# Performance work log

Hardware: AMD Instinct MI355X
Metric: run time of the kernel (lower is better)

## Reference

```python
import jax, jax.numpy as jnp
import numpy as np

N, E, B = 65536, 524288, 256
FEAT, EMB, NH, NB, NC = 64, 128, 4, 2, 4
OUT = EMB // NH
SLOPE = 0.01  # LeakyReLU negative_slope used everywhere in the module


def lrelu(x):
    return jnp.where(x > 0, x, SLOPE * x)


def seg_softmax(logits, seg, nseg, mask):
    # PyG softmax(src, batch): exp(x - segment_max) / (segment_sum + 1e-16)
    z = jnp.where(mask, logits, -jnp.inf)
    m = jax.ops.segment_max(z, seg, num_segments=nseg)
    m = jnp.where(jnp.isfinite(m), m, 0.0)
    e = jnp.exp(z - m[seg])
    s = jax.ops.segment_sum(e, seg, num_segments=nseg)
    return e / (s[seg] + 1e-16)


def topk_pool(x, seg, w, min_score, nseg):
    # PyG TopKPooling with min_score: score = softmax(x.w, batch);
    # keep nodes with score > min(min_score, per-graph max - 1e-7); x_out = x*score.
    score = x @ w  # [N]
    sm = seg_softmax(score, seg, nseg, jnp.ones(score.shape, bool))
    smax = jax.ops.segment_max(sm, seg, num_segments=nseg)
    thr = jnp.minimum(smax - 1e-7, min_score)
    keep = sm > thr[seg]
    xp = jnp.where(keep[:, None], x * sm[:, None], 0.0)
    return xp, keep


def graph_conv_max(x, src, dst, emask, Wrel, Wroot, b, n):
    # PyG GraphConv(aggr='max'): out = Wrel @ max_{j in N(i)} x_j + Wroot @ x_i + b
    msg = jnp.where(emask[:, None], x[src], -jnp.inf)  # [E, d]
    agg = jax.ops.segment_max(msg, dst, num_segments=n)
    agg = jnp.where(jnp.isfinite(agg), agg, 0.0)  # nodes with no in-edges -> 0 (PyG scatter fill)
    return agg @ Wrel.T + x @ Wroot.T + b


def batchnorm(x, g, b):
    # training-mode BatchNorm1d: batch statistics, biased variance, eps=1e-5
    mu = x.mean(0)
    var = x.var(0)
    return g * (x - mu) * jax.lax.rsqrt(var + 1e-5) + b


def setup_inputs() -> dict:
    key = jax.random.key(0)
    ks = jax.random.split(key, 16)
    s_feat = np.float32(1.0 / np.sqrt(FEAT))
    s_emb = np.float32(1.0 / np.sqrt(EMB))
    return {
        "x": jax.random.normal(ks[0], (N, FEAT), jnp.float32),
        "edge_index": jax.random.randint(ks[1], (2, E), 0, N, jnp.int32),
        "batch": (jnp.arange(N, dtype=jnp.int32) // (N // B)).astype(jnp.int32),
        "W_rel0": jax.random.normal(ks[2], (EMB, FEAT), jnp.float32) * s_feat,
        "W_root0": jax.random.normal(ks[3], (EMB, FEAT), jnp.float32) * s_feat,
        "b0": jnp.zeros((EMB,), jnp.float32),
        "bn0_g": jnp.ones((EMB,), jnp.float32),
        "bn0_b": jnp.zeros((EMB,), jnp.float32),
        "blk_pool_w": jax.random.normal(ks[4], (NB, NH, EMB), jnp.float32) * s_emb,
        "blk_Wrel": jax.random.normal(ks[5], (NB, NH, OUT, EMB), jnp.float32) * s_emb,
        "blk_Wroot": jax.random.normal(ks[6], (NB, NH, OUT, EMB), jnp.float32) * s_emb,
        "blk_b": jnp.zeros((NB, NH, OUT), jnp.float32),
        "blk_bn_g": jnp.ones((NB, EMB), jnp.float32),
        "blk_bn_b": jnp.zeros((NB, EMB), jnp.float32),
        "cls_pool_w": jax.random.normal(ks[7], (NC, EMB), jnp.float32) * s_emb,
        "cls_gW1": jax.random.normal(ks[8], (NC, EMB, EMB), jnp.float32) * s_emb,
        "cls_gb1": jnp.zeros((NC, EMB), jnp.float32),
        "cls_gW2": jax.random.normal(ks[9], (NC, EMB), jnp.float32) * s_emb,
        "cls_gb2": jnp.zeros((NC,), jnp.float32),
        "cls_fW1": jax.random.normal(ks[10], (NC, EMB, EMB), jnp.float32) * s_emb,
        "cls_fb1": jnp.zeros((NC, EMB), jnp.float32),
        "cls_fW2": jax.random.normal(ks[11], (NC, EMB), jnp.float32) * s_emb,
        "cls_fb2": jnp.zeros((NC,), jnp.float32),
        "batch_size": B,
    }


def reference(x, edge_index, batch, W_rel0, W_root0, b0, bn0_g, bn0_b,
              blk_pool_w, blk_Wrel, blk_Wroot, blk_b, blk_bn_g, blk_bn_b,
              cls_pool_w, cls_gW1, cls_gb1, cls_gW2, cls_gb2,
              cls_fW1, cls_fb1, cls_fW2, cls_fb2, batch_size):
    n = x.shape[0]
    src, dst = edge_index[0], edge_index[1]
    all_e = jnp.ones(src.shape, bool)
    # conv0 -> leaky_relu -> bn0
    h = lrelu(graph_conv_max(x, src, dst, all_e, W_rel0, W_root0, b0, n))
    cur = batchnorm(h, bn0_g, bn0_b)
    # multi-head blocks: pool (min_score=0.7) -> GraphConv(max) per head, scatter
    # back to original node slots, concat heads, bn, residual 0.5*(x + 0.5*bn(new))
    for bi in range(NB):
        heads = []
        for hi in range(NH):
            xp, keep = topk_pool(cur, batch, blk_pool_w[bi, hi], 0.7, batch_size)
            emask = keep[src] & keep[dst]
            o = lrelu(graph_conv_max(xp, src, dst, emask,
                                     blk_Wrel[bi, hi], blk_Wroot[bi, hi],
                                     blk_b[bi, hi], n))
            heads.append(jnp.where(keep[:, None], o, 0.0))
        new = batchnorm(jnp.concatenate(heads, axis=-1), blk_bn_g[bi], blk_bn_b[bi])
        cur = 0.5 * (cur + 0.5 * new)
    # classification heads: pool (min_score=0.8) -> GlobalAttention -> MLP -> 1
    outs = []
    for c in range(NC):
        xp, keep = topk_pool(cur, batch, cls_pool_w[c], 0.8, batch_size)
        gate = lrelu(xp @ cls_gW1[c].T + cls_gb1[c]) @ cls_gW2[c] + cls_gb2[c]  # [N]
        a = seg_softmax(gate, batch, batch_size, keep)
        pooled = jax.ops.segment_sum(a[:, None] * xp, batch, num_segments=batch_size)  # [B, EMB]
        y = lrelu(pooled @ cls_fW1[c].T + cls_fb1[c]) @ cls_fW2[c] + cls_fb2[c]  # [B]
        outs.append(y)
    logits = jnp.stack(outs, axis=-1)  # [B, NC]
    return jax.nn.log_softmax(logits, axis=-1)
```

## Files before the change

kernel.cpp:

```cpp
#include <hip/hip_runtime.h>
#include <math.h>

#define NN 65536
#define NE 524288
#define NG 256
#define SLOPE 0.01f
#define CAP 131072

__device__ __forceinline__ float lrelu(float v){ return v > 0.f ? v : SLOPE*v; }

__device__ __forceinline__ float blockMax4(float v, float* s4){
  #pragma unroll
  for(int o=32;o>0;o>>=1) v = fmaxf(v, __shfl_down(v, o, 64));
  int t = threadIdx.x;
  __syncthreads();
  if((t&63)==0) s4[t>>6] = v;
  __syncthreads();
  return fmaxf(fmaxf(s4[0], s4[1]), fmaxf(s4[2], s4[3]));
}
__device__ __forceinline__ float blockSum4(float v, float* s4){
  #pragma unroll
  for(int o=32;o>0;o>>=1) v += __shfl_down(v, o, 64);
  int t = threadIdx.x;
  __syncthreads();
  if((t&63)==0) s4[t>>6] = v;
  __syncthreads();
  return (s4[0]+s4[1])+(s4[2]+s4[3]);
}

__global__ __launch_bounds__(256) void k_count(const int* __restrict__ ei, int* __restrict__ deg){
  int e = blockIdx.x*256 + threadIdx.x;
  if(e < NE) atomicAdd(&deg[ei[NE + e]], 1);
}

__global__ __launch_bounds__(1024) void k_scan(const int* __restrict__ deg,
      int* __restrict__ offs, int* __restrict__ cursor){
  __shared__ int part[1024];
  int t = threadIdx.x;
  const int4* d4 = (const int4*)(deg + t*64);
  int4 buf[16];
  int s=0;
  #pragma unroll
  for(int i=0;i<16;i++){ buf[i]=d4[i]; s += buf[i].x+buf[i].y+buf[i].z+buf[i].w; }
  part[t]=s;
  __syncthreads();
  for(int off=1; off<1024; off<<=1){
    int v = (t>=off)? part[t-off] : 0;
    __syncthreads();
    part[t] += v;
    __syncthreads();
  }
  int run = (t==0)? 0 : part[t-1];
  #pragma unroll
  for(int i=0;i<16;i++){
    int4 d = buf[i];
    int4 o;
    o.x = run; run += d.x;
    o.y = run; run += d.y;
    o.z = run; run += d.z;
    o.w = run; run += d.w;
    ((int4*)(offs + t*64))[i] = o;
    ((int4*)(cursor + t*64))[i] = o;
  }
  if(t==1023) offs[NN] = run;
}

__global__ __launch_bounds__(256) void k_scatter(const int* __restrict__ ei,
      int* __restrict__ cursor, int* __restrict__ csr){
  int e = blockIdx.x*256 + threadIdx.x;
  if(e < NE){
    int d = ei[NE + e];
    int p = atomicAdd(&cursor[d], 1);
    csr[p] = ei[e];
  }
}

__global__ __launch_bounds__(256) void k_agg0(const float* __restrict__ x,
    const int* __restrict__ offs, const int* __restrict__ csr, float* __restrict__ agg0){
  int tid = blockIdx.x*256 + threadIdx.x;
  int node = tid>>4, q = tid&15;
  int e0 = offs[node], e1 = offs[node+1];
  float4 acc = make_float4(0.f,0.f,0.f,0.f);
  if(e0 < e1){
    acc = make_float4(-INFINITY,-INFINITY,-INFINITY,-INFINITY);
    int e = e0;
    for(; e+7 < e1; e += 8){
      int si[8];
      #pragma unroll
      for(int u=0;u<8;u++) si[u] = csr[e+u];
      float4 v[8];
      #pragma unroll
      for(int u=0;u<8;u++) v[u] = ((const float4*)x)[si[u]*16 + q];
      #pragma unroll
      for(int u=0;u<8;u++){
        acc.x=fmaxf(acc.x,v[u].x); acc.y=fmaxf(acc.y,v[u].y);
        acc.z=fmaxf(acc.z,v[u].z); acc.w=fmaxf(acc.w,v[u].w);
      }
    }
    for(; e < e1; e++){
      int s0 = csr[e];
      float4 v0 = ((const float4*)x)[s0*16 + q];
      acc.x=fmaxf(acc.x,v0.x); acc.y=fmaxf(acc.y,v0.y);
      acc.z=fmaxf(acc.z,v0.z); acc.w=fmaxf(acc.w,v0.w);
    }
  }
  ((float4*)agg0)[node*16 + q] = acc;
}

__global__ __launch_bounds__(256, 2) void k_conv0mm(
    const float* __restrict__ agg0, const float* __restrict__ x,
    const float* __restrict__ Wrel, const float* __restrict__ Wroot,
    const float* __restrict__ b0, float* __restrict__ cur,
    float* __restrict__ bnsum, float* __restrict__ bnsq){
  __shared__ float4 As[2048];
  __shared__ float4 Ws[2048];
  const int t = threadIdx.x;
  const int tn = t & 15;
  const int tc = t >> 4;
  float acc[8][8];
  #pragma unroll
  for(int i=0;i<8;i++)
    #pragma unroll
    for(int j=0;j<8;j++) acc[i][j]=0.f;

  const size_t tileoff = (size_t)blockIdx.x * 8192;
  #pragma unroll 1
  for(int ch=0; ch<2; ch++){
    const float4* gA = (const float4*)((ch==0? agg0 : x) + tileoff);
    const float4* gW = (const float4*)(ch==0? Wrel : Wroot);
    __syncthreads();
    #pragma unroll
    for(int i=0;i<8;i++){
      int idx = t + i*256;
      int n = idx>>4, k4 = idx&15;
      int sw = n*16 + ((k4 + (n>>3))&15);
      As[sw] = gA[idx];
      Ws[sw] = gW[idx];
    }
    __syncthreads();
    #pragma unroll 1
    for(int k4=0;k4<16;k4++){
      float4 a4[8];
      #pragma unroll
      for(int i=0;i<8;i++) a4[i] = As[(tn*8+i)*16 + ((k4+tn)&15)];
      #pragma unroll
      for(int j=0;j<8;j++){
        float4 w4 = Ws[(tc*8+j)*16 + ((k4+tc)&15)];
        #pragma unroll
        for(int i=0;i<8;i++){
          acc[i][j] = fmaf(a4[i].x, w4.x, acc[i][j]);
          acc[i][j] = fmaf(a4[i].y, w4.y, acc[i][j]);
          acc[i][j] = fmaf(a4[i].z, w4.z, acc[i][j]);
          acc[i][j] = fmaf(a4[i].w, w4.w, acc[i][j]);
        }
      }
    }
  }

  float bj[8];
  #pragma unroll
  for(int j=0;j<8;j++) bj[j] = b0[tc*8+j];
  float cs[8], cq[8];
  #pragma unroll
  for(int j=0;j<8;j++){ cs[j]=0.f; cq[j]=0.f; }
  const int nbase = blockIdx.x*128;
  #pragma unroll
  for(int i=0;i<8;i++){
    int node = nbase + tn*8 + i;
    float v[8];
    #pragma unroll
    for(int j=0;j<8;j++){
      v[j] = lrelu(acc[i][j] + bj[j]);
      cs[j] += v[j]; cq[j] += v[j]*v[j];
    }
    float4 o0 = make_float4(v[0],v[1],v[2],v[3]);
    float4 o1 = make_float4(v[4],v[5],v[6],v[7]);
    ((float4*)cur)[node*32 + tc*2 + 0] = o0;
    ((float4*)cur)[node*32 + tc*2 + 1] = o1;
  }
  __syncthreads();
  float* reds = (float*)As;
  float* redq = (float*)Ws;
  #pragma unroll
  for(int j=0;j<8;j++){
    reds[(tc*8+j)*16 + tn] = cs[j];
    redq[(tc*8+j)*16 + tn] = cq[j];
  }
  __syncthreads();
  if(t<128){
    float S=0.f, Q=0.f;
    #pragma unroll
    for(int i=0;i<16;i++){ S += reds[t*16+i]; Q += redq[t*16+i]; }
    atomicAdd(&bnsum[t], S);
    atomicAdd(&bnsq[t], Q);
  }
}

__global__ __launch_bounds__(256) void k_scores(const float* __restrict__ cur0,
    const float* __restrict__ bns0, const float* __restrict__ bnq0,
    const float* __restrict__ g0,
    const float* __restrict__ pw0, const float* __restrict__ pw1,
    const float* __restrict__ pwc,
    float* __restrict__ scores0, float* __restrict__ pre1, float* __restrict__ pre2){
  __shared__ __align__(16) float w[12][128];
  __shared__ float sc0s[128];
  const int t = threadIdx.x;
  if(t<128){
    float mu = bns0[t]*(1.0f/NN);
    float var = bnq0[t]*(1.0f/NN) - mu*mu;
    sc0s[t] = g0[t]*rsqrtf(var+1e-5f);
  }
  __syncthreads();
  for(int i=t;i<512;i+=256){
    int h=i>>7, j=i&127;
    float s = sc0s[j];
    w[h][j]   = pw0[i]*s;
    w[4+h][j] = pw1[i]*(0.5f*s);
    w[8+h][j] = pwc[i]*(0.25f*s);
  }
  __syncthreads();
  const int tid = blockIdx.x*256 + t;
  const int n = tid>>5, k = tid&31;
  float4 v = ((const float4*)cur0)[tid];
  float a[12];
  #pragma unroll
  for(int q=0;q<12;q++){
    float4 wv = *(const float4*)&w[q][k*4];
    a[q] = v.x*wv.x + v.y*wv.y + v.z*wv.z + v.w*wv.w;
  }
  #pragma unroll
  for(int o=16;o>0;o>>=1){
    #pragma unroll
    for(int q=0;q<12;q++) a[q] += __shfl_down(a[q], o, 32);
  }
  if(k==0){
    ((float4*)scores0)[n] = make_float4(a[0],a[1],a[2],a[3]);
    ((float4*)pre1)[n]    = make_float4(a[4],a[5],a[6],a[7]);
    ((float4*)pre2)[n]    = make_float4(a[8],a[9],a[10],a[11]);
  }
}

__global__ __launch_bounds__(256) void k_poolsel(const float* __restrict__ scores,
    float minscore, float* __restrict__ sm4, unsigned char* __restrict__ keep,
    int* __restrict__ cnt, int* __restrict__ wl, int* __restrict__ idx){
  __shared__ float red[4];
  const int t = threadIdx.x, g = blockIdx.x, n = g*256 + t;
  float4 s4 = ((const float4*)scores)[n];
  float scv[4] = {s4.x, s4.y, s4.z, s4.w};
  float4 smout;
  unsigned kb = 0;
  #pragma unroll 1
  for(int h=0;h<4;h++){
    float m = blockMax4(scv[h], red);
    float e = expf(scv[h]-m);
    float ssum = blockSum4(e, red);
    float sm = e/(ssum + 1e-16f);
    float smax = blockMax4(sm, red);
    float thr = fminf(smax - 1e-7f, minscore);
    ((float*)&smout)[h] = sm;
    if(sm > thr){
      int p = atomicAdd(cnt, 1);
      if(p < CAP){
        kb |= (1u<<h);
        wl[p] = (h<<16) | n;
        idx[n*4+h] = p;
      }
    }
  }
  __syncthreads();
  ((float4*)sm4)[n] = smout;
  keep[n] = (unsigned char)kb;
}

__global__ __launch_bounds__(256) void k_blockconv0(const float* __restrict__ cur0,
    const int* __restrict__ offs, const int* __restrict__ csr,
    const unsigned char* __restrict__ keep, const float* __restrict__ sm4,
    const int* __restrict__ cnt, const int* __restrict__ wl,
    const float* __restrict__ Wrel, const float* __restrict__ Wroot,
    const float* __restrict__ bias,
    float* __restrict__ new1c, float* __restrict__ bnsum, float* __restrict__ bnsq,
    const float* __restrict__ bns0, const float* __restrict__ bnq0,
    const float* __restrict__ g0, const float* __restrict__ b0bn){
  __shared__ __align__(16) float aggs[8][128];
  __shared__ __align__(16) float xps[8][128];
  __shared__ __align__(16) float scv[128];
  __shared__ __align__(16) float ofv[128];
  const int t = threadIdx.x, grp = t>>5, lane = t&31;
  if(t<128){
    float mu = bns0[t]*(1.0f/NN);
    float var = bnq0[t]*(1.0f/NN) - mu*mu;
    float sv = g0[t]*rsqrtf(var+1e-5f);
    scv[t]=sv; ofv[t]=b0bn[t]-mu*sv;
  }
  __syncthreads();
  const float4 s4l = *(const float4*)&scv[lane*4];
  const float4 o4l = *(const float4*)&ofv[lane*4];
  int total = *cnt; if(total > CAP) total = CAP;
  for(int item = blockIdx.x*8 + grp; item < total; item += gridDim.x*8){
    const int wv = wl[item];
    const int h = wv>>16, n = wv & 0xFFFF;
    const float smn = sm4[n*4+h];
    const int e0 = offs[n], e1 = offs[n+1];
    float4 acc = make_float4(-INFINITY,-INFINITY,-INFINITY,-INFINITY);
    bool any = false;
    for(int e=e0;e<e1;e++){
      int s = csr[e];
      if((keep[s]>>h)&1){
        any = true;
        float sv = sm4[s*4+h];
        float4 v = ((const float4*)cur0)[s*32 + lane];
        v.x = (v.x*s4l.x + o4l.x)*sv; v.y = (v.y*s4l.y + o4l.y)*sv;
        v.z = (v.z*s4l.z + o4l.z)*sv; v.w = (v.w*s4l.w + o4l.w)*sv;
        acc.x = fmaxf(acc.x, v.x); acc.y = fmaxf(acc.y, v.y);
        acc.z = fmaxf(acc.z, v.z); acc.w = fmaxf(acc.w, v.w);
      }
    }
    if(!any) acc = make_float4(0.f,0.f,0.f,0.f);
    *(float4*)&aggs[grp][lane*4] = acc;
    float4 xv = ((const float4*)cur0)[n*32 + lane];
    xv.x = (xv.x*s4l.x + o4l.x)*smn; xv.y = (xv.y*s4l.y + o4l.y)*smn;
    xv.z = (xv.z*s4l.z + o4l.z)*smn; xv.w = (xv.w*s4l.w + o4l.w)*smn;
    *(float4*)&xps[grp][lane*4] = xv;
    const float* Wr = Wrel  + (size_t)(h*32+lane)*128;
    const float* Wo = Wroot + (size_t)(h*32+lane)*128;
    float o = bias[h*32+lane];
    for(int k=0;k<32;k++){
      float4 a  = *(const float4*)&aggs[grp][k*4];
      float4 xx = *(const float4*)&xps[grp][k*4];
      float4 wr = ((const float4*)Wr)[k];
      float4 wo = ((const float4*)Wo)[k];
      o += a.x*wr.x + a.y*wr.y + a.z*wr.z + a.w*wr.w;
      o += xx.x*wo.x + xx.y*wo.y + xx.z*wo.z + xx.w*wo.w;
    }
    o = lrelu(o);
    new1c[(size_t)item*32 + lane] = o;
    atomicAdd(&bnsum[h*32+lane], o);
    atomicAdd(&bnsq[h*32+lane], o*o);
  }
}

__global__ __launch_bounds__(256) void k_poolsel1(
    const float* __restrict__ pre1, float* __restrict__ pre2,
    const int* __restrict__ cnt0, const int* __restrict__ wl0,
    const float* __restrict__ new1c,
    const float* __restrict__ bnsA, const float* __restrict__ bnqA,
    const float* __restrict__ g1v,
    const float* __restrict__ pw1, const float* __restrict__ pwc,
    float minscore, float* __restrict__ sm4out, unsigned char* __restrict__ keep1,
    int* __restrict__ cnt1, int* __restrict__ wl1, int* __restrict__ idx1){
  __shared__ float red[4];
  __shared__ float s1s[128];
  __shared__ __align__(16) float w1s[4][128];
  __shared__ __align__(16) float wcs[4][128];
  __shared__ float patch1[256][4];
  const int t = threadIdx.x, g = blockIdx.x;
  if(t<128){
    float mu = bnsA[t]*(1.0f/NN);
    float var = bnqA[t]*(1.0f/NN) - mu*mu;
    s1s[t] = g1v[t]*rsqrtf(var+1e-5f);
  }
  for(int i=t;i<512;i+=256){ w1s[i>>7][i&127]=pw1[i]; wcs[i>>7][i&127]=pwc[i]; }
  #pragma unroll
  for(int h=0;h<4;h++) patch1[t][h]=0.f;
  __syncthreads();
  int total0 = *cnt0; if(total0 > CAP) total0 = CAP;
  for(int i=t; i<total0; i+=256){
    int wv = wl0[i];
    int n = wv & 0xFFFF, hp = wv>>16;
    if((n>>8)==g){
      int nl = n & 255;
      float d[4]={0.f,0.f,0.f,0.f}, d2[4]={0.f,0.f,0.f,0.f};
      for(int l=0;l<32;l++){
        int j = hp*32+l;
        float base = new1c[(size_t)i*32+l] * s1s[j];
        #pragma unroll
        for(int h=0;h<4;h++){ d[h]+=base*w1s[h][j]; d2[h]+=base*wcs[h][j]; }
      }
      #pragma unroll
      for(int h=0;h<4;h++){
        atomicAdd(&patch1[nl][h], 0.25f*d[h]);
        atomicAdd(&pre2[n*4+h], 0.125f*d2[h]);
      }
    }
  }
  __syncthreads();
  const int n = g*256 + t;
  float4 p4 = ((const float4*)pre1)[n];
  float scv[4] = {p4.x+patch1[t][0], p4.y+patch1[t][1],
                  p4.z+patch1[t][2], p4.w+patch1[t][3]};
  float4 smout;
  unsigned kb = 0;
  #pragma unroll 1
  for(int h=0;h<4;h++){
    float m = blockMax4(scv[h], red);
    float e = expf(scv[h]-m);
    float ssum = blockSum4(e, red);
    float sm = e/(ssum + 1e-16f);
    float smax = blockMax4(sm, red);
    float thr = fminf(smax - 1e-7f, minscore);
    ((float*)&smout)[h] = sm;
    if(sm > thr){
      int p = atomicAdd(cnt1, 1);
      if(p < CAP){
        kb |= (1u<<h);
        wl1[p] = (h<<16) | n;
        idx1[n*4+h] = p;
      }
    }
  }
  __syncthreads();
  ((float4*)sm4out)[n] = smout;
  keep1[n] = (unsigned char)kb;
}

__global__ __launch_bounds__(256) void k_blockconv1(const float* __restrict__ cur0,
    const int* __restrict__ offs, const int* __restrict__ csr,
    const unsigned char* __restrict__ keep0, const int* __restrict__ idx0,
    const float* __restrict__ new1c,
    const unsigned char* __restrict__ keep1, const float* __restrict__ sm41,
    const int* __restrict__ cnt1, const int* __restrict__ wl1,
    const float* __restrict__ Wrel, const float* __restrict__ Wroot,
    const float* __restrict__ bias,
    float* __restrict__ new2c, float* __restrict__ bnsum, float* __restrict__ bnsq,
    const float* __restrict__ bns0, const float* __restrict__ bnq0,
    const float* __restrict__ g0, const float* __restrict__ b0bn,
    const float* __restrict__ bnsA, const float* __restrict__ bnqA,
    const float* __restrict__ g1v, const float* __restrict__ b1v){
  __shared__ __align__(16) float aggs[8][128];
  __shared__ __align__(16) float xps[8][128];
  __shared__ __align__(16) float sc0s[128], of0s[128], s1s[128], o1s[128];
  const int t = threadIdx.x, grp = t>>5, lane = t&31;
  if(t<128){
    float mu = bns0[t]*(1.0f/NN);
    float var = bnq0[t]*(1.0f/NN) - mu*mu;
    float sv = g0[t]*rsqrtf(var+1e-5f);
    sc0s[t]=sv; of0s[t]=b0bn[t]-mu*sv;
    float mu1 = bnsA[t]*(1.0f/NN);
    float var1 = bnqA[t]*(1.0f/NN) - mu1*mu1;
    float s1 = g1v[t]*rsqrtf(var1+1e-5f);
    s1s[t]=s1; o1s[t]=b1v[t]-mu1*s1;
  }
  __syncthreads();
  const float4 s0l = *(const float4*)&sc0s[lane*4];
  const float4 o0l = *(const float4*)&of0s[lane*4];
  const float4 s1l = *(const float4*)&s1s[lane*4];
  const float4 o1l = *(const float4*)&o1s[lane*4];
  const int hb = lane>>3;
  int total = *cnt1; if(total > CAP) total = CAP;
  for(int item = blockIdx.x*8 + grp; item < total; item += gridDim.x*8){
    const int wv = wl1[item];
    const int h = wv>>16, n = wv & 0xFFFF;
    const float smn = sm41[n*4+h];
    const int e0 = offs[n], e1 = offs[n+1];
    float4 acc = make_float4(-INFINITY,-INFINITY,-INFINITY,-INFINITY);
    bool any = false;
    for(int e=e0;e<e1;e++){
      int s = csr[e];
      if((keep1[s]>>h)&1){
        any = true;
        float sv = sm41[s*4+h];
        float4 c0 = ((const float4*)cur0)[s*32 + lane];
        float4 v;
        v.x = 0.5f*(s0l.x*c0.x+o0l.x) + 0.25f*o1l.x;
        v.y = 0.5f*(s0l.y*c0.y+o0l.y) + 0.25f*o1l.y;
        v.z = 0.5f*(s0l.z*c0.z+o0l.z) + 0.25f*o1l.z;
        v.w = 0.5f*(s0l.w*c0.w+o0l.w) + 0.25f*o1l.w;
        if((keep0[s]>>hb)&1){
          float4 nv = ((const float4*)(new1c + (size_t)idx0[s*4+hb]*32))[lane&7];
          v.x += 0.25f*s1l.x*nv.x; v.y += 0.25f*s1l.y*nv.y;
          v.z += 0.25f*s1l.z*nv.z; v.w += 0.25f*s1l.w*nv.w;
        }
        v.x*=sv; v.y*=sv; v.z*=sv; v.w*=sv;
        acc.x = fmaxf(acc.x, v.x); acc.y = fmaxf(acc.y, v.y);
        acc.z = fmaxf(acc.z, v.z); acc.w = fmaxf(acc.w, v.w);
      }
    }
    if(!any) acc = make_float4(0.f,0.f,0.f,0.f);
    *(float4*)&aggs[grp][lane*4] = acc;
    {
      float4 c0 = ((const float4*)cur0)[n*32 + lane];
      float4 v;
      v.x = 0.5f*(s0l.x*c0.x+o0l.x) + 0.25f*o1l.x;
      v.y = 0.5f*(s0l.y*c0.y+o0l.y) + 0.25f*o1l.y;
      v.z = 0.5f*(s0l.z*c0.z+o0l.z) + 0.25f*o1l.z;
      v.w = 0.5f*(s0l.w*c0.w+o0l.w) + 0.25f*o1l.w;
      if((keep0[n]>>hb)&1){
        float4 nv = ((const float4*)(new1c + (size_t)idx0[n*4+hb]*32))[lane&7];
        v.x += 0.25f*s1l.x*nv.x; v.y += 0.25f*s1l.y*nv.y;
        v.z += 0.25f*s1l.z*nv.z; v.w += 0.25f*s1l.w*nv.w;
      }
      v.x*=smn; v.y*=smn; v.z*=smn; v.w*=smn;
      *(float4*)&xps[grp][lane*4] = v;
    }
    const float* Wr = Wrel  + (size_t)(h*32+lane)*128;
    const float* Wo = Wroot + (size_t)(h*32+lane)*128;
    float o = bias[h*32+lane];
    for(int k=0;k<32;k++){
      float4 a  = *(const float4*)&aggs[grp][k*4];
      float4 xx = *(const float4*)&xps[grp][k*4];
      float4 wr = ((const float4*)Wr)[k];
      float4 wo = ((const float4*)Wo)[k];
      o += a.x*wr.x + a.y*wr.y + a.z*wr.z + a.w*wr.w;
      o += xx.x*wo.x + xx.y*wo.y + xx.z*wo.z + xx.w*wo.w;
    }
    o = lrelu(o);
    new2c[(size_t)item*32 + lane] = o;
    atomicAdd(&bnsum[h*32+lane], o);
    atomicAdd(&bnsq[h*32+lane], o*o);
  }
}

__global__ __launch_bounds__(256) void k_cls2(const float* __restrict__ cur0,
    const unsigned char* __restrict__ keep0, const int* __restrict__ idx0,
    const float* __restrict__ new1c,
    const unsigned char* __restrict__ keep1, const int* __restrict__ idx1,
    const float* __restrict__ new2c,
    const float* __restrict__ pre2, const int* __restrict__ cnt1,
    const int* __restrict__ wl1, const float* __restrict__ pwc,
    const float* __restrict__ bns0, const float* __restrict__ bnq0,
    const float* __restrict__ g0, const float* __restrict__ b0bn,
    const float* __restrict__ bnsA, const float* __restrict__ bnqA,
    const float* __restrict__ g1v, const float* __restrict__ b1v,
    const float* __restrict__ bnsB, const float* __restrict__ bnqB,
    const float* __restrict__ g2v, const float* __restrict__ b2v,
    const float* __restrict__ gW1, const float* __restrict__ gb1,
    const float* __restrict__ gW2, const float* __restrict__ gb2,
    const float* __restrict__ fW1, const float* __restrict__ fb1,
    const float* __restrict__ fW2, const float* __restrict__ fb2,
    float* __restrict__ yws){
  __shared__ float red[4];
  __shared__ float sc0s[128], of0s[128], s1s[128], o1s[128], s2s[128], o2s[128];
  __shared__ float wc[128];
  __shared__ float patch[256];
  __shared__ int keptL[256];
  __shared__ float keptS[256];
  __shared__ float gateL[256];
  __shared__ __align__(16) float xk[128];
  __shared__ __align__(16) float pooled[128];
  __shared__ int nkept;
  const int t = threadIdx.x;
  const int g = blockIdx.x >> 2, c = blockIdx.x & 3;
  if(t<128){
    float mu = bns0[t]*(1.0f/NN);
    float var = bnq0[t]*(1.0f/NN) - mu*mu;
    float sv = g0[t]*rsqrtf(var+1e-5f);
    sc0s[t]=sv; of0s[t]=b0bn[t]-mu*sv;
    float mu1 = bnsA[t]*(1.0f/NN);
    float var1 = bnqA[t]*(1.0f/NN) - mu1*mu1;
    float s1 = g1v[t]*rsqrtf(var1+1e-5f);
    s1s[t]=s1; o1s[t]=b1v[t]-mu1*s1;
    float mu2 = bnsB[t]*(1.0f/NN);
    float var2 = bnqB[t]*(1.0f/NN) - mu2*mu2;
    float s2 = g2v[t]*rsqrtf(var2+1e-5f);
    s2s[t]=s2; o2s[t]=b2v[t]-mu2*s2;
    wc[t] = pwc[c*128+t];
  }
  patch[t]=0.f;
  __syncthreads();
  int total1 = *cnt1; if(total1 > CAP) total1 = CAP;
  for(int i=t; i<total1; i+=256){
    int wv = wl1[i];
    int n = wv & 0xFFFF, hp = wv>>16;
    if((n>>8)==g){
      float d=0.f;
      for(int l=0;l<32;l++){
        int j = hp*32+l;
        d += new2c[(size_t)i*32+l]*s2s[j]*wc[j];
      }
      atomicAdd(&patch[n&255], 0.25f*d);
    }
  }
  __syncthreads();
  const int n = g*256 + t;
  float sc = pre2[n*4 + c] + patch[t];
  float m = blockMax4(sc, red);
  float e = expf(sc-m);
  float ssum = blockSum4(e, red);
  float sm = e/(ssum+1e-16f);
  float smax = blockMax4(sm, red);
  float thr = fminf(smax - 1e-7f, 0.8f);
  if(t==0) nkept = 0;
  __syncthreads();
  if(sm > thr){
    int p = atomicAdd(&nkept,1);
    keptL[p]=t; keptS[p]=sm;
  }
  __syncthreads();
  const int K = nkept;
  for(int k=0;k<K;k++){
    int ln = keptL[k]; float sv = keptS[k];
    int nn = g*256 + ln;
    if(t<32){
      float4 c0 = ((const float4*)cur0)[nn*32 + t];
      float4 s0l = *(const float4*)&sc0s[t*4];
      float4 o0l = *(const float4*)&of0s[t*4];
      float4 s1l = *(const float4*)&s1s[t*4];
      float4 o1l = *(const float4*)&o1s[t*4];
      float4 s2l = *(const float4*)&s2s[t*4];
      float4 o2l = *(const float4*)&o2s[t*4];
      int hb = t>>3;
      float4 v1;
      v1.x = 0.5f*(s0l.x*c0.x+o0l.x) + 0.25f*o1l.x;
      v1.y = 0.5f*(s0l.y*c0.y+o0l.y) + 0.25f*o1l.y;
      v1.z = 0.5f*(s0l.z*c0.z+o0l.z) + 0.25f*o1l.z;
      v1.w = 0.5f*(s0l.w*c0.w+o0l.w) + 0.25f*o1l.w;
      if((keep0[nn]>>hb)&1){
        float4 nv = ((const float4*)(new1c + (size_t)idx0[nn*4+hb]*32))[t&7];
        v1.x += 0.25f*s1l.x*nv.x; v1.y += 0.25f*s1l.y*nv.y;
        v1.z += 0.25f*s1l.z*nv.z; v1.w += 0.25f*s1l.w*nv.w;
      }
      float4 v2;
      v2.x = 0.5f*v1.x + 0.25f*o2l.x;
      v2.y = 0.5f*v1.y + 0.25f*o2l.y;
      v2.z = 0.5f*v1.z + 0.25f*o2l.z;
      v2.w = 0.5f*v1.w + 0.25f*o2l.w;
      if((keep1[nn]>>hb)&1){
        float4 nv = ((const float4*)(new2c + (size_t)idx1[nn*4+hb]*32))[t&7];
        v2.x += 0.25f*s2l.x*nv.x; v2.y += 0.25f*s2l.y*nv.y;
        v2.z += 0.25f*s2l.z*nv.z; v2.w += 0.25f*s2l.w*nv.w;
      }
      v2.x*=sv; v2.y*=sv; v2.z*=sv; v2.w*=sv;
      *(float4*)&xk[t*4] = v2;
    }
    __syncthreads();
    float part = 0.f;
    if(t<128){
      const float* W = gW1 + (size_t)c*16384 + (size_t)t*128;
      float a = gb1[c*128+t];
      for(int f=0;f<32;f++){
        float4 xv = *(const float4*)&xk[f*4];
        float4 wv = ((const float4*)W)[f];
        a += xv.x*wv.x + xv.y*wv.y + xv.z*wv.z + xv.w*wv.w;
      }
      part = lrelu(a) * gW2[c*128+t];
    }
    float gs = blockSum4(part, red);
    if(t==0) gateL[k] = gs + gb2[c];
    __syncthreads();
  }
  float gv = (t<K)? gateL[t] : -INFINITY;
  float gm = blockMax4(gv, red);
  float ge = (t<K)? expf(gv-gm) : 0.f;
  float gsum = blockSum4(ge, red);
  if(t<K) gateL[t] = ge/(gsum+1e-16f);
  __syncthreads();
  if(t<128){
    int hb = t>>5, l = t&31;
    float acc = 0.f;
    for(int k=0;k<K;k++){
      int nn = g*256 + keptL[k];
      float c0 = cur0[(size_t)nn*128 + t];
      float v1 = 0.5f*(sc0s[t]*c0 + of0s[t]) + 0.25f*o1s[t];
      if((keep0[nn]>>hb)&1) v1 += 0.25f*s1s[t]*new1c[(size_t)idx0[nn*4+hb]*32 + l];
      float v2 = 0.5f*v1 + 0.25f*o2s[t];
      if((keep1[nn]>>hb)&1) v2 += 0.25f*s2s[t]*new2c[(size_t)idx1[nn*4+hb]*32 + l];
      acc += gateL[k]*keptS[k]*v2;
    }
    pooled[t]=acc;
  }
  __syncthreads();
  float part2=0.f;
  if(t<128){
    const float* F = fW1 + (size_t)c*16384 + (size_t)t*128;
    float a = fb1[c*128+t];
    for(int f=0;f<32;f++){
      float4 xv = *(const float4*)&pooled[f*4];
      float4 wv = ((const float4*)F)[f];
      a += xv.x*wv.x + xv.y*wv.y + xv.z*wv.z + xv.w*wv.w;
    }
    part2 = lrelu(a) * fW2[c*128+t];
  }
  float ysum = blockSum4(part2, red);
  if(t==0) yws[g*4+c] = ysum + fb2[c];
}

__global__ __launch_bounds__(256) void k_clsfin(const float* __restrict__ yws,
                                                float* __restrict__ out){
  const int g = threadIdx.x;
  float4 y = ((const float4*)yws)[g];
  float m = fmaxf(fmaxf(y.x,y.y), fmaxf(y.z,y.w));
  float l = logf(expf(y.x-m)+expf(y.y-m)+expf(y.z-m)+expf(y.w-m));
  ((float4*)out)[g] = make_float4(y.x-m-l, y.y-m-l, y.z-m-l, y.w-m-l);
}

extern "C" void kernel_launch(void* const* d_in, const int* in_sizes, int n_in,
                              void* d_out, int out_size, void* d_ws, size_t ws_size,
                              hipStream_t stream){
  (void)in_sizes; (void)n_in; (void)out_size; (void)ws_size;
  const float* x     = (const float*)d_in[0];
  const int*   ei    = (const int*)d_in[1];
  const float* Wrel0 = (const float*)d_in[3];
  const float* Wroot0= (const float*)d_in[4];
  const float* b0    = (const float*)d_in[5];
  const float* bn0g  = (const float*)d_in[6];
  const float* bn0b  = (const float*)d_in[7];
  const float* bpw   = (const float*)d_in[8];
  const float* bWrel = (const float*)d_in[9];
  const float* bWroot= (const float*)d_in[10];
  const float* bbv   = (const float*)d_in[11];
  const float* bbng  = (const float*)d_in[12];
  const float* bbnb  = (const float*)d_in[13];
  const float* cpw   = (const float*)d_in[14];
  const float* gW1   = (const float*)d_in[15];
  const float* gb1   = (const float*)d_in[16];
  const float* gW2   = (const float*)d_in[17];
  const float* gb2   = (const float*)d_in[18];
  const float* fW1   = (const float*)d_in[19];
  const float* fb1   = (const float*)d_in[20];
  const float* fW2   = (const float*)d_in[21];
  const float* fb2   = (const float*)d_in[22];

  char* ws = (char*)d_ws;
  float* cur0  = (float*)(ws + 0);
  float* new1c = (float*)(ws + 33554432ull);
  float* new2c = (float*)(ws + 50331648ull);
  float* agg0  = new2c;
  int*   csr   = (int*)(ws + 67108864ull);
  float* scores0=(float*)(ws + 69206016ull);
  float* sm40  = scores0;
  float* pre1  = (float*)(ws + 70254592ull);
  float* sm41  = pre1;
  float* pre2  = (float*)(ws + 71303168ull);
  int*   wl0   = (int*)(ws + 72351744ull);
  int*   wl1   = (int*)(ws + 72876032ull);
  int*   offs  = (int*)(ws + 73400320ull);
  int*   cursor= (int*)(ws + 73666560ull);
  unsigned char* keep0 = (unsigned char*)(ws + 73928704ull);
  unsigned char* keep1 = (unsigned char*)(ws + 73994240ull);
  int*   idx0  = (int*)(ws + 74059776ull);
  int*   idx1  = (int*)(ws + 75108352ull);
  char*  Z     = ws + 76156928ull;
  int*   deg   = (int*)Z;
  float* bnsum0= (float*)(Z + 262144);
  float* bnsq0 = (float*)(Z + 262656);
  float* bnA   = (float*)(Z + 263168);
  float* bqA   = (float*)(Z + 263680);
  float* bnB   = (float*)(Z + 264192);
  float* bqB   = (float*)(Z + 264704);
  int*   cnt0  = (int*)(Z + 265216);
  int*   cnt1  = (int*)(Z + 265220);
  float* yws   = (float*)(Z + 266240);

  hipMemsetAsync(Z, 0, 270336, stream);
  hipMemsetAsync(idx0, 0xFF, 2097152, stream);

  k_count  <<<2048,256,0,stream>>>(ei, deg);
  k_scan   <<<1,1024,0,stream>>>(deg, offs, cursor);
  k_scatter<<<2048,256,0,stream>>>(ei, cursor, csr);

  k_agg0    <<<4096,256,0,stream>>>(x, offs, csr, agg0);
  k_conv0mm <<<512,256,0,stream>>>(agg0, x, Wrel0, Wroot0, b0, cur0, bnsum0, bnsq0);

  k_scores<<<8192,256,0,stream>>>(cur0, bnsum0, bnsq0, bn0g,
                                  bpw, bpw + 512, cpw, scores0, pre1, pre2);

  k_poolsel<<<256,256,0,stream>>>(scores0, 0.7f, sm40, keep0, cnt0, wl0, idx0);

  k_blockconv0<<<256,256,0,stream>>>(cur0, offs, csr, keep0, sm40, cnt0, wl0,
                                     bWrel, bWroot, bbv, new1c, bnA, bqA,
                                     bnsum0, bnsq0, bn0g, bn0b);

  k_poolsel1<<<256,256,0,stream>>>(pre1, pre2, cnt0, wl0, new1c,
                                   bnA, bqA, bbng,
                                   bpw + 512, cpw,
                                   0.7f, sm41, keep1, cnt1, wl1, idx1);

  k_blockconv1<<<256,256,0,stream>>>(cur0, offs, csr, keep0, idx0, new1c,
                                     keep1, sm41, cnt1, wl1,
                                     bWrel + 16384, bWroot + 16384, bbv + 128,
                                     new2c, bnB, bqB,
                                     bnsum0, bnsq0, bn0g, bn0b,
                                     bnA, bqA, bbng, bbnb);

  k_cls2<<<1024,256,0,stream>>>(cur0, keep0, idx0, new1c, keep1, idx1, new2c,
                                pre2, cnt1, wl1, cpw,
                                bnsum0, bnsq0, bn0g, bn0b,
                                bnA, bqA, bbng, bbnb,
                                bnB, bqB, bbng + 128, bbnb + 128,
                                gW1, gb1, gW2, gb2, fW1, fb1, fW2, fb2, yws);
  k_clsfin<<<1,256,0,stream>>>(yws, (float*)d_out);
}
```

Measured before the change: 384.1 us.

## Use wave-per-head pool selection with head-major index maps; drop keep bitmasks

Pool selection now assigns one 64-lane wave per head and uses wave-level xor shuffles instead of four serialized block-wide reductions. The keep bitmask plus node-major idx array is replaced by a head-major int map that stores -1 for dropped nodes. This removes the separate 0xFF memset, and the conv and classifier kernels now look up keep status and slot in one load. Separately, the conv0 GEMM no longer stages weights in shared memory and reads them directly from global/L1, which halves its LDS footprint but may add global load latency in the inner loop.

```diff
diff --git a/kernel.cpp b/kernel.cpp
--- a/kernel.cpp
+++ b/kernel.cpp
@@ -113,7 +113,6 @@
     const float* __restrict__ b0, float* __restrict__ cur,
     float* __restrict__ bnsum, float* __restrict__ bnsq){
   __shared__ float4 As[2048];
-  __shared__ float4 Ws[2048];
   const int t = threadIdx.x;
   const int tn = t & 15;
   const int tc = t >> 4;
@@ -133,9 +132,7 @@
     for(int i=0;i<8;i++){
       int idx = t + i*256;
       int n = idx>>4, k4 = idx&15;
-      int sw = n*16 + ((k4 + (n>>3))&15);
-      As[sw] = gA[idx];
-      Ws[sw] = gW[idx];
+      As[n*16 + ((k4 + (n>>3))&15)] = gA[idx];
     }
     __syncthreads();
     #pragma unroll 1
@@ -145,7 +142,7 @@
       for(int i=0;i<8;i++) a4[i] = As[(tn*8+i)*16 + ((k4+tn)&15)];
       #pragma unroll
       for(int j=0;j<8;j++){
-        float4 w4 = Ws[(tc*8+j)*16 + ((k4+tc)&15)];
+        float4 w4 = gW[(tc*8+j)*16 + k4];
         #pragma unroll
         for(int i=0;i<8;i++){
           acc[i][j] = fmaf(a4[i].x, w4.x, acc[i][j]);
@@ -180,7 +177,7 @@
   }
   __syncthreads();
   float* reds = (float*)As;
-  float* redq = (float*)Ws;
+  float* redq = ((float*)As) + 2048;
   #pragma unroll
   for(int j=0;j<8;j++){
     reds[(tc*8+j)*16 + tn] = cs[j];
@@ -240,41 +237,47 @@
   }
 }
 
-__global__ __launch_bounds__(256) void k_poolsel(const float* __restrict__ scores,
-    float minscore, float* __restrict__ sm4, unsigned char* __restrict__ keep,
-    int* __restrict__ cnt, int* __restrict__ wl, int* __restrict__ idx){
-  __shared__ float red[4];
-  const int t = threadIdx.x, g = blockIdx.x, n = g*256 + t;
-  float4 s4 = ((const float4*)scores)[n];
-  float scv[4] = {s4.x, s4.y, s4.z, s4.w};
-  float4 smout;
-  unsigned kb = 0;
-  #pragma unroll 1
-  for(int h=0;h<4;h++){
-    float m = blockMax4(scv[h], red);
-    float e = expf(scv[h]-m);
-    float ssum = blockSum4(e, red);
-    float sm = e/(ssum + 1e-16f);
-    float smax = blockMax4(sm, red);
-    float thr = fminf(smax - 1e-7f, minscore);
-    ((float*)&smout)[h] = sm;
-    if(sm > thr){
+__global__ __launch_bounds__(256) void k_poolselW(const float* __restrict__ scores,
+    float minscore, float* __restrict__ sm4, int* __restrict__ cnt,
+    int* __restrict__ wl, int* __restrict__ idxP){
+  const int t = threadIdx.x, g = blockIdx.x;
+  const int h = t>>6, l = t&63;
+  const int n0 = g*256;
+  float s[4];
+  #pragma unroll
+  for(int i=0;i<4;i++) s[i] = scores[(size_t)(n0 + l + i*64)*4 + h];
+  float m = fmaxf(fmaxf(s[0],s[1]),fmaxf(s[2],s[3]));
+  #pragma unroll
+  for(int o=32;o>0;o>>=1) m = fmaxf(m, __shfl_xor(m, o, 64));
+  float e[4], es=0.f;
+  #pragma unroll
+  for(int i=0;i<4;i++){ e[i]=expf(s[i]-m); es+=e[i]; }
+  #pragma unroll
+  for(int o=32;o>0;o>>=1) es += __shfl_xor(es, o, 64);
+  float inv = 1.f/(es+1e-16f);
+  float sm[4];
+  float mx = -INFINITY;
+  #pragma unroll
+  for(int i=0;i<4;i++){ sm[i]=e[i]*inv; mx=fmaxf(mx,sm[i]); }
+  #pragma unroll
+  for(int o=32;o>0;o>>=1) mx = fmaxf(mx, __shfl_xor(mx, o, 64));
+  float thr = fminf(mx - 1e-7f, minscore);
+  #pragma unroll
+  for(int i=0;i<4;i++){
+    int n = n0 + l + i*64;
+    sm4[(size_t)n*4 + h] = sm[i];
+    int slot = -1;
+    if(sm[i] > thr){
       int p = atomicAdd(cnt, 1);
-      if(p < CAP){
-        kb |= (1u<<h);
-        wl[p] = (h<<16) | n;
-        idx[n*4+h] = p;
-      }
-    }
-  }
-  __syncthreads();
-  ((float4*)sm4)[n] = smout;
-  keep[n] = (unsigned char)kb;
+      if(p < CAP){ slot = p; wl[p] = (h<<16) | n; }
+    }
+    idxP[(size_t)h*NN + n] = slot;
+  }
 }
 
 __global__ __launch_bounds__(256) void k_blockconv0(const float* __restrict__ cur0,
     const int* __restrict__ offs, const int* __restrict__ csr,
-    const unsigned char* __restrict__ keep, const float* __restrict__ sm4,
+    const int* __restrict__ idxP, const float* __restrict__ sm4,
     const int* __restrict__ cnt, const int* __restrict__ wl,
     const float* __restrict__ Wrel, const float* __restrict__ Wroot,
     const float* __restrict__ bias,
@@ -299,15 +302,16 @@
   for(int item = blockIdx.x*8 + grp; item < total; item += gridDim.x*8){
     const int wv = wl[item];
     const int h = wv>>16, n = wv & 0xFFFF;
-    const float smn = sm4[n*4+h];
+    const size_t hn = (size_t)h*NN;
+    const float smn = sm4[(size_t)n*4+h];
     const int e0 = offs[n], e1 = offs[n+1];
     float4 acc = make_float4(-INFINITY,-INFINITY,-INFINITY,-INFINITY);
     bool any = false;
     for(int e=e0;e<e1;e++){
       int s = csr[e];
-      if((keep[s]>>h)&1){
+      if(idxP[hn + s] >= 0){
         any = true;
-        float sv = sm4[s*4+h];
+        float sv = sm4[(size_t)s*4+h];
         float4 v = ((const float4*)cur0)[s*32 + lane];
         v.x = (v.x*s4l.x + o4l.x)*sv; v.y = (v.y*s4l.y + o4l.y)*sv;
         v.z = (v.z*s4l.z + o4l.z)*sv; v.w = (v.w*s4l.w + o4l.w)*sv;
@@ -346,9 +350,8 @@
     const float* __restrict__ bnsA, const float* __restrict__ bnqA,
     const float* __restrict__ g1v,
     const float* __restrict__ pw1, const float* __restrict__ pwc,
-    float minscore, float* __restrict__ sm4out, unsigned char* __restrict__ keep1,
-    int* __restrict__ cnt1, int* __restrict__ wl1, int* __restrict__ idx1){
-  __shared__ float red[4];
+    float minscore, float* __restrict__ sm4out,
+    int* __restrict__ cnt1, int* __restrict__ wl1, int* __restrict__ idx1P){
   __shared__ float s1s[128];
   __shared__ __align__(16) float w1s[4][128];
   __shared__ __align__(16) float wcs[4][128];
@@ -384,40 +387,47 @@
     }
   }
   __syncthreads();
-  const int n = g*256 + t;
-  float4 p4 = ((const float4*)pre1)[n];
-  float scv[4] = {p4.x+patch1[t][0], p4.y+patch1[t][1],
-                  p4.z+patch1[t][2], p4.w+patch1[t][3]};
-  float4 smout;
-  unsigned kb = 0;
-  #pragma unroll 1
-  for(int h=0;h<4;h++){
-    float m = blockMax4(scv[h], red);
-    float e = expf(scv[h]-m);
-    float ssum = blockSum4(e, red);
-    float sm = e/(ssum + 1e-16f);
-    float smax = blockMax4(sm, red);
-    float thr = fminf(smax - 1e-7f, minscore);
-    ((float*)&smout)[h] = sm;
-    if(sm > thr){
+  const int h = t>>6, l = t&63;
+  const int n0 = g*256;
+  float s[4];
+  #pragma unroll
+  for(int i=0;i<4;i++){
+    int nl = l + i*64;
+    s[i] = pre1[(size_t)(n0+nl)*4 + h] + patch1[nl][h];
+  }
+  float m = fmaxf(fmaxf(s[0],s[1]),fmaxf(s[2],s[3]));
+  #pragma unroll
+  for(int o=32;o>0;o>>=1) m = fmaxf(m, __shfl_xor(m, o, 64));
+  float e[4], es=0.f;
+  #pragma unroll
+  for(int i=0;i<4;i++){ e[i]=expf(s[i]-m); es+=e[i]; }
+  #pragma unroll
+  for(int o=32;o>0;o>>=1) es += __shfl_xor(es, o, 64);
+  float inv = 1.f/(es+1e-16f);
+  float sm[4];
+  float mx = -INFINITY;
+  #pragma unroll
+  for(int i=0;i<4;i++){ sm[i]=e[i]*inv; mx=fmaxf(mx,sm[i]); }
+  #pragma unroll
+  for(int o=32;o>0;o>>=1) mx = fmaxf(mx, __shfl_xor(mx, o, 64));
+  float thr = fminf(mx - 1e-7f, minscore);
+  #pragma unroll
+  for(int i=0;i<4;i++){
+    int n = n0 + l + i*64;
+    sm4out[(size_t)n*4 + h] = sm[i];
+    int slot = -1;
+    if(sm[i] > thr){
       int p = atomicAdd(cnt1, 1);
-      if(p < CAP){
-        kb |= (1u<<h);
-        wl1[p] = (h<<16) | n;
-        idx1[n*4+h] = p;
-      }
-    }
-  }
-  __syncthreads();
-  ((float4*)sm4out)[n] = smout;
-  keep1[n] = (unsigned char)kb;
+      if(p < CAP){ slot = p; wl1[p] = (h<<16) | n; }
+    }
+    idx1P[(size_t)h*NN + n] = slot;
+  }
 }
 
 __global__ __launch_bounds__(256) void k_blockconv1(const float* __restrict__ cur0,
     const int* __restrict__ offs, const int* __restrict__ csr,
-    const unsigned char* __restrict__ keep0, const int* __restrict__ idx0,
-    const float* __restrict__ new1c,
-    const unsigned char* __restrict__ keep1, const float* __restrict__ sm41,
+    const int* __restrict__ idx0P, const float* __restrict__ new1c,
+    const int* __restrict__ idx1P, const float* __restrict__ sm41,
     const int* __restrict__ cnt1, const int* __restrict__ wl1,
     const float* __restrict__ Wrel, const float* __restrict__ Wroot,
     const float* __restrict__ bias,
@@ -446,27 +456,30 @@
   const float4 s1l = *(const float4*)&s1s[lane*4];
   const float4 o1l = *(const float4*)&o1s[lane*4];
   const int hb = lane>>3;
+  const size_t hbn = (size_t)hb*NN;
   int total = *cnt1; if(total > CAP) total = CAP;
   for(int item = blockIdx.x*8 + grp; item < total; item += gridDim.x*8){
     const int wv = wl1[item];
     const int h = wv>>16, n = wv & 0xFFFF;
-    const float smn = sm41[n*4+h];
+    const size_t hn = (size_t)h*NN;
+    const float smn = sm41[(size_t)n*4+h];
     const int e0 = offs[n], e1 = offs[n+1];
     float4 acc = make_float4(-INFINITY,-INFINITY,-INFINITY,-INFINITY);
     bool any = false;
     for(int e=e0;e<e1;e++){
       int s = csr[e];
-      if((keep1[s]>>h)&1){
+      if(idx1P[hn + s] >= 0){
         any = true;
-        float sv = sm41[s*4+h];
+        float sv = sm41[(size_t)s*4+h];
         float4 c0 = ((const float4*)cur0)[s*32 + lane];
         float4 v;
         v.x = 0.5f*(s0l.x*c0.x+o0l.x) + 0.25f*o1l.x;
         v.y = 0.5f*(s0l.y*c0.y+o0l.y) + 0.25f*o1l.y;
         v.z = 0.5f*(s0l.z*c0.z+o0l.z) + 0.25f*o1l.z;
         v.w = 0.5f*(s0l.w*c0.w+o0l.w) + 0.25f*o1l.w;
-        if((keep0[s]>>hb)&1){
-          float4 nv = ((const float4*)(new1c + (size_t)idx0[s*4+hb]*32))[lane&7];
+        int i0 = idx0P[hbn + s];
+        if(i0 >= 0){
+          float4 nv = ((const float4*)(new1c + (size_t)i0*32))[lane&7];
           v.x += 0.25f*s1l.x*nv.x; v.y += 0.25f*s1l.y*nv.y;
           v.z += 0.25f*s1l.z*nv.z; v.w += 0.25f*s1l.w*nv.w;
         }
@@ -484,8 +497,9 @@
       v.y = 0.5f*(s0l.y*c0.y+o0l.y) + 0.25f*o1l.y;
       v.z = 0.5f*(s0l.z*c0.z+o0l.z) + 0.25f*o1l.z;
       v.w = 0.5f*(s0l.w*c0.w+o0l.w) + 0.25f*o1l.w;
-      if((keep0[n]>>hb)&1){
-        float4 nv = ((const float4*)(new1c + (size_t)idx0[n*4+hb]*32))[lane&7];
+      int i0 = idx0P[hbn + n];
+      if(i0 >= 0){
+        float4 nv = ((const float4*)(new1c + (size_t)i0*32))[lane&7];
         v.x += 0.25f*s1l.x*nv.x; v.y += 0.25f*s1l.y*nv.y;
         v.z += 0.25f*s1l.z*nv.z; v.w += 0.25f*s1l.w*nv.w;
       }
@@ -511,10 +525,8 @@
 }
 
 __global__ __launch_bounds__(256) void k_cls2(const float* __restrict__ cur0,
-    const unsigned char* __restrict__ keep0, const int* __restrict__ idx0,
-    const float* __restrict__ new1c,
-    const unsigned char* __restrict__ keep1, const int* __restrict__ idx1,
-    const float* __restrict__ new2c,
+    const int* __restrict__ idx0P, const float* __restrict__ new1c,
+    const int* __restrict__ idx1P, const float* __restrict__ new2c,
     const float* __restrict__ pre2, const int* __restrict__ cnt1,
     const int* __restrict__ wl1, const float* __restrict__ pwc,
     const float* __restrict__ bns0, const float* __restrict__ bnq0,
@@ -604,8 +616,9 @@
       v1.y = 0.5f*(s0l.y*c0.y+o0l.y) + 0.25f*o1l.y;
       v1.z = 0.5f*(s0l.z*c0.z+o0l.z) + 0.25f*o1l.z;
       v1.w = 0.5f*(s0l.w*c0.w+o0l.w) + 0.25f*o1l.w;
-      if((keep0[nn]>>hb)&1){
-        float4 nv = ((const float4*)(new1c + (size_t)idx0[nn*4+hb]*32))[t&7];
+      int i0 = idx0P[(size_t)hb*NN + nn];
+      if(i0 >= 0){
+        float4 nv = ((const float4*)(new1c + (size_t)i0*32))[t&7];
         v1.x += 0.25f*s1l.x*nv.x; v1.y += 0.25f*s1l.y*nv.y;
         v1.z += 0.25f*s1l.z*nv.z; v1.w += 0.25f*s1l.w*nv.w;
       }
@@ -614,8 +627,9 @@
       v2.y = 0.5f*v1.y + 0.25f*o2l.y;
       v2.z = 0.5f*v1.z + 0.25f*o2l.z;
       v2.w = 0.5f*v1.w + 0.25f*o2l.w;
-      if((keep1[nn]>>hb)&1){
-        float4 nv = ((const float4*)(new2c + (size_t)idx1[nn*4+hb]*32))[t&7];
+      int i1 = idx1P[(size_t)hb*NN + nn];
+      if(i1 >= 0){
+        float4 nv = ((const float4*)(new2c + (size_t)i1*32))[t&7];
         v2.x += 0.25f*s2l.x*nv.x; v2.y += 0.25f*s2l.y*nv.y;
         v2.z += 0.25f*s2l.z*nv.z; v2.w += 0.25f*s2l.w*nv.w;
       }
@@ -651,9 +665,11 @@
       int nn = g*256 + keptL[k];
       float c0 = cur0[(size_t)nn*128 + t];
       float v1 = 0.5f*(sc0s[t]*c0 + of0s[t]) + 0.25f*o1s[t];
-      if((keep0[nn]>>hb)&1) v1 += 0.25f*s1s[t]*new1c[(size_t)idx0[nn*4+hb]*32 + l];
+      int i0 = idx0P[(size_t)hb*NN + nn];
+      if(i0 >= 0) v1 += 0.25f*s1s[t]*new1c[(size_t)i0*32 + l];
       float v2 = 0.5f*v1 + 0.25f*o2s[t];
-      if((keep1[nn]>>hb)&1) v2 += 0.25f*s2s[t]*new2c[(size_t)idx1[nn*4+hb]*32 + l];
+      int i1 = idx1P[(size_t)hb*NN + nn];
+      if(i1 >= 0) v2 += 0.25f*s2s[t]*new2c[(size_t)i1*32 + l];
       acc += gateL[k]*keptS[k]*v2;
     }
     pooled[t]=acc;
@@ -725,11 +741,9 @@
   int*   wl1   = (int*)(ws + 72876032ull);
   int*   offs  = (int*)(ws + 73400320ull);
   int*   cursor= (int*)(ws + 73666560ull);
-  unsigned char* keep0 = (unsigned char*)(ws + 73928704ull);
-  unsigned char* keep1 = (unsigned char*)(ws + 73994240ull);
-  int*   idx0  = (int*)(ws + 74059776ull);
-  int*   idx1  = (int*)(ws + 75108352ull);
-  char*  Z     = ws + 76156928ull;
+  int*   idx0P = (int*)(ws + 73928704ull);
+  int*   idx1P = (int*)(ws + 74977280ull);
+  char*  Z     = ws + 76025856ull;
   int*   deg   = (int*)Z;
   float* bnsum0= (float*)(Z + 262144);
   float* bnsq0 = (float*)(Z + 262656);
@@ -742,7 +756,6 @@
   float* yws   = (float*)(Z + 266240);
 
   hipMemsetAsync(Z, 0, 270336, stream);
-  hipMemsetAsync(idx0, 0xFF, 2097152, stream);
 
   k_count  <<<2048,256,0,stream>>>(ei, deg);
   k_scan   <<<1,1024,0,stream>>>(deg, offs, cursor);
@@ -754,25 +767,25 @@
   k_scores<<<8192,256,0,stream>>>(cur0, bnsum0, bnsq0, bn0g,
                                   bpw, bpw + 512, cpw, scores0, pre1, pre2);
 
-  k_poolsel<<<256,256,0,stream>>>(scores0, 0.7f, sm40, keep0, cnt0, wl0, idx0);
-
-  k_blockconv0<<<256,256,0,stream>>>(cur0, offs, csr, keep0, sm40, cnt0, wl0,
+  k_poolselW<<<256,256,0,stream>>>(scores0, 0.7f, sm40, cnt0, wl0, idx0P);
+
+  k_blockconv0<<<256,256,0,stream>>>(cur0, offs, csr, idx0P, sm40, cnt0, wl0,
                                      bWrel, bWroot, bbv, new1c, bnA, bqA,
                                      bnsum0, bnsq0, bn0g, bn0b);
 
   k_poolsel1<<<256,256,0,stream>>>(pre1, pre2, cnt0, wl0, new1c,
                                    bnA, bqA, bbng,
                                    bpw + 512, cpw,
-                                   0.7f, sm41, keep1, cnt1, wl1, idx1);
-
-  k_blockconv1<<<256,256,0,stream>>>(cur0, offs, csr, keep0, idx0, new1c,
-                                     keep1, sm41, cnt1, wl1,
+                                   0.7f, sm41, cnt1, wl1, idx1P);
+
+  k_blockconv1<<<256,256,0,stream>>>(cur0, offs, csr, idx0P, new1c,
+                                     idx1P, sm41, cnt1, wl1,
                                      bWrel + 16384, bWroot + 16384, bbv + 128,
                                      new2c, bnB, bqB,
                                      bnsum0, bnsq0, bn0g, bn0b,
                                      bnA, bqA, bbng, bbnb);
 
-  k_cls2<<<1024,256,0,stream>>>(cur0, keep0, idx0, new1c, keep1, idx1, new2c,
+  k_cls2<<<1024,256,0,stream>>>(cur0, idx0P, new1c, idx1P, new2c,
                                 pre2, cnt1, wl1, cpw,
                                 bnsum0, bnsq0, bn0g, bn0b,
                                 bnA, bqA, bbng, bbnb,
```

New measurement: 379.5 us. About the same (-1.2%).
